# Kernel tuning notes

Hardware: AMD Instinct MI355X
Metric: run time of the kernel (lower is better)

The kernel has to match this reference:

```python
import jax, jax.numpy as jnp
import numpy as np

VOCAB, DIM, SEQ, DEPTH, WS, MULT = 32, 256, 8192, 6, 512, 4
BATCH = 2
NEG = -1e9  # mask fill value


def setup_inputs():
    key = jax.random.key(0)
    ks = jax.random.split(key, 8)
    L, d, h = DEPTH, DIM, DIM * MULT
    s = 0.02
    return {
        "tokens": jax.random.randint(ks[0], (BATCH, SEQ), 0, VOCAB),
        "embed": jax.random.normal(ks[1], (VOCAB, d)) * s,
        "ff_ln_s": jnp.ones((L, d)),
        "ff_ln_b": jnp.zeros((L, d)),
        "w1": jax.random.normal(ks[2], (L, d, h)) * s,
        "b1": jnp.zeros((L, h)),
        "w2": jax.random.normal(ks[3], (L, h, d)) * s,
        "b2": jnp.zeros((L, d)),
        "lnf_s": jnp.ones((d,)),
        "lnf_b": jnp.zeros((d,)),
        "w_out": jax.random.normal(ks[4], (d, VOCAB)) * s,
        "b_out": jnp.zeros((VOCAB,)),
    }


def layer_norm(x, s, b, eps=1e-5):
    m = jnp.mean(x, axis=-1, keepdims=True)
    v = jnp.var(x, axis=-1, keepdims=True)
    return (x - m) * jax.lax.rsqrt(v + eps) * s + b


def rotate_half(x):
    x1, x2 = jnp.split(x, 2, axis=-1)
    return jnp.concatenate([-x2, x1], axis=-1)


def local_attn(x, ws):
    # lucidrains LocalAttention: causal, look_backward=1, look_forward=0,
    # exact_windowsize=True, rotary pos emb on q/k. q = k = v = x (no projections).
    b, n, d = x.shape
    inv_freq = 1.0 / (10000.0 ** (jnp.arange(0, d, 2, dtype=jnp.float32) / d))
    t = jnp.arange(n, dtype=jnp.float32)
    fr = t[:, None] * inv_freq[None, :]
    fr = jnp.concatenate([fr, fr], axis=-1)  # (n, d)
    qk = x * jnp.cos(fr) + rotate_half(x) * jnp.sin(fr)  # rotary applied to q and k (identical)
    w = n // ws
    bq = qk.reshape(b, w, ws, d)
    bk = bq  # q == k here
    bv = x.reshape(b, w, ws, d)
    # look_around: each window sees [previous window, current window]
    pk = jnp.pad(bk, ((0, 0), (1, 0), (0, 0), (0, 0)))[:, :-1]
    pv = jnp.pad(bv, ((0, 0), (1, 0), (0, 0), (0, 0)))[:, :-1]
    bk2 = jnp.concatenate([pk, bk], axis=2)  # (b, w, 2*ws, d)
    bv2 = jnp.concatenate([pv, bv], axis=2)
    tq = jnp.arange(n).reshape(w, ws)
    tp = jnp.pad(tq, ((1, 0), (0, 0)), constant_values=-1)[:-1]
    tk = jnp.concatenate([tp, tq], axis=1)  # (w, 2*ws), -1 marks pad
    allowed = (
        (tk[:, None, :] >= 0)
        & (tq[:, :, None] >= tk[:, None, :])          # causal
        & (tq[:, :, None] <= tk[:, None, :] + ws)     # exact windowsize (look_backward=1)
    )
    sim = jnp.einsum("bwid,bwjd->bwij", bq, bk2) * (d ** -0.5)
    sim = jnp.where(allowed[None], sim, NEG)
    attn = jax.nn.softmax(sim, axis=-1)
    out = jnp.einsum("bwij,bwjd->bwid", attn, bv2)
    return out.reshape(b, n, d)


def reference(tokens, embed, ff_ln_s, ff_ln_b, w1, b1, w2, b2, lnf_s, lnf_b, w_out, b_out):
    x = embed[tokens]  # (b, n, d)
    for i in range(DEPTH):
        x = x + local_attn(x, WS)
        h = layer_norm(x, ff_ln_s[i], ff_ln_b[i])
        h = jax.nn.gelu(h @ w1[i] + b1[i], approximate=False)
        x = x + (h @ w2[i] + b2[i])
    return layer_norm(x, lnf_s, lnf_b) @ w_out + b_out  # (b, n, vocab)
```

## Files before the change

### kernel.cpp

```cpp
#include <hip/hip_runtime.h>
#include <hip/hip_bf16.h>
#include <math.h>

#define BATCH 2
#define SEQL 8192
#define DD 256
#define HDIM 1024
#define NLAYER 6
#define WSZ 512
#define NVOCAB 32
#define NTOK (BATCH*SEQL)
#define PLN (DD*HDIM)

typedef unsigned short u16;
typedef __attribute__((ext_vector_type(8))) short bf16x8;
typedef __attribute__((ext_vector_type(4))) float f32x4;

union B8 { uint4 u; bf16x8 b; ushort s[8]; uint w[4]; };

__device__ inline float bf2f(u16 v){
  unsigned int u = ((unsigned int)v) << 16;
  return __uint_as_float(u);
}
__device__ inline u16 f2bf(float f){
  unsigned int u = __float_as_uint(f);
  u += 0x7fff + ((u >> 16) & 1);
  return (u16)(u >> 16);
}

__device__ __forceinline__ void gload16(const void* g, void* l){
  __builtin_amdgcn_global_load_lds(
      (const __attribute__((address_space(1))) unsigned int*)g,
      (__attribute__((address_space(3))) unsigned int*)l, 16, 0, 0);
}

__global__ void k_tables(float* __restrict__ ct, float* __restrict__ st){
  int idx = blockIdx.x * 256 + threadIdx.x;
  if (idx >= SEQL * 128) return;
  int t = idx >> 7, i = idx & 127;
  float freq = expf(-((float)i / 128.0f) * 9.210340371976184f);
  float fr = (float)t * freq;
  ct[idx] = cosf(fr);
  st[idx] = sinf(fr);
}

__global__ void k_embed(const int* __restrict__ tokens, const float* __restrict__ emb,
                        float* __restrict__ x){
  int idx = blockIdx.x * 256 + threadIdx.x;
  int bt = idx >> 6, dv = (idx & 63) << 2;
  int tok = tokens[bt];
  *(float4*)(x + bt * DD + dv) = *(const float4*)(emb + tok * DD + dv);
}

__global__ void k_rope(const float* __restrict__ x, const float* __restrict__ ct,
                       const float* __restrict__ st, u16* __restrict__ qk,
                       u16* __restrict__ xv){
  int idx = blockIdx.x * 256 + threadIdx.x;
  int bt = idx >> 5, iv = (idx & 31) << 2;
  int t = bt & (SEQL - 1);
  const float* xr = x + bt * DD;
  float4 x1 = *(const float4*)(xr + iv);
  float4 x2 = *(const float4*)(xr + 128 + iv);
  float4 c = *(const float4*)(ct + t * 128 + iv);
  float4 s = *(const float4*)(st + t * 128 + iv);
  ushort4 q1, q2, v1, v2;
  q1.x = f2bf(x1.x * c.x - x2.x * s.x);  q2.x = f2bf(x2.x * c.x + x1.x * s.x);
  q1.y = f2bf(x1.y * c.y - x2.y * s.y);  q2.y = f2bf(x2.y * c.y + x1.y * s.y);
  q1.z = f2bf(x1.z * c.z - x2.z * s.z);  q2.z = f2bf(x2.z * c.z + x1.z * s.z);
  q1.w = f2bf(x1.w * c.w - x2.w * s.w);  q2.w = f2bf(x2.w * c.w + x1.w * s.w);
  v1.x = f2bf(x1.x); v1.y = f2bf(x1.y); v1.z = f2bf(x1.z); v1.w = f2bf(x1.w);
  v2.x = f2bf(x2.x); v2.y = f2bf(x2.y); v2.z = f2bf(x2.z); v2.w = f2bf(x2.w);
  *(ushort4*)(qk + bt * DD + iv)       = q1;
  *(ushort4*)(qk + bt * DD + 128 + iv) = q2;
  *(ushort4*)(xv + bt * DD + iv)       = v1;
  *(ushort4*)(xv + bt * DD + 128 + iv) = v2;
}

__global__ void __launch_bounds__(512, 2) k_attn2(const u16* __restrict__ qk,
                                                  const u16* __restrict__ xv,
                                                  const float* __restrict__ x,
                                                  float* __restrict__ y,
                                                  const float* __restrict__ g,
                                                  const float* __restrict__ b,
                                                  u16* __restrict__ lnx,
                                                  int fuse){
  __shared__ char smem[131072];
  float* redbuf = (float*)smem;

  const int tid = threadIdx.x;
  const int lane = tid & 63;
  const int w = tid >> 6;
  const int qh = w >> 1, kh = w & 1;
  const int l15 = lane & 15, lg = lane >> 4;

  const int qg = (blockIdx.x & 7) * 32 + (blockIdx.x >> 3);
  const int qb = qg * 64;
  const int t0 = qb & (SEQL - 1);
  const size_t bbase = (size_t)(qb >> 13) << 13;

  uint4 qf[8];
  {
    const u16* qr = qk + (size_t)(qb + qh*16 + l15) * DD + lg*4;
    #pragma unroll
    for (int s = 0; s < 8; ++s){
      uint2 a = *(const uint2*)(qr + s*32);
      uint2 bq = *(const uint2*)(qr + s*32 + 16);
      qf[s] = make_uint4(a.x, a.y, bq.x, bq.y);
    }
  }

  f32x4 oacc[16];
  #pragma unroll
  for (int d = 0; d < 16; ++d) oacc[d] = (f32x4){0.f, 0.f, 0.f, 0.f};
  float lacc = 0.f;

  const int p0 = (t0 >= WSZ) ? (t0 - WSZ) : 0;
  const int ntile = ((t0 - p0) >> 6) + 1;

  const int sk15 = tid & 15, skt = (tid >> 4) & 3, sc = tid >> 6;
  const int sdh = tid & 31, sk0 = (tid >> 5) * 4;
  const int vkhw = sk0 >> 5, vh = (sk0 >> 4) & 1, vlgw = (sk0 >> 2) & 3;

  uint4 kreg[4];
  uint  vreg[4][4];

  {
    const u16* sb = qk + (bbase + (size_t)p0 + skt*16 + sk15) * DD;
    #pragma unroll
    for (int u = 0; u < 4; ++u) kreg[u] = *(const uint4*)(sb + u*64 + sc*8);
    #pragma unroll
    for (int u = 0; u < 4; ++u){
      int d0 = sdh*2 + u*64;
      const u16* vb = xv + (bbase + (size_t)p0 + sk0) * DD + d0;
      vreg[u][0] = *(const uint*)(vb);
      vreg[u][1] = *(const uint*)(vb + DD);
      vreg[u][2] = *(const uint*)(vb + 2*DD);
      vreg[u][3] = *(const uint*)(vb + 3*DD);
    }
  }
  #pragma unroll
  for (int u = 0; u < 4; ++u){
    int d0 = u*64 + sc*8;
    int s = d0 >> 5, r = d0 & 31;
    int h = r >> 4, lgw = (r & 15) >> 2;
    int rec = ((s*4 + skt)*4 + lgw)*16 + sk15;
    char* wp = smem + rec*16 + h*8;
    *(uint2*)wp         = make_uint2(kreg[u].x, kreg[u].y);
    *(uint2*)(wp + 256) = make_uint2(kreg[u].z, kreg[u].w);
  }
  #pragma unroll
  for (int u = 0; u < 4; ++u){
    int d0 = sdh*2 + u*64;
    uint a0 = vreg[u][0], a1 = vreg[u][1], a2 = vreg[u][2], a3 = vreg[u][3];
    uint w0 = (a0 & 0xffffu) | (a1 << 16);
    uint w1 = (a2 & 0xffffu) | (a3 << 16);
    uint w2 = (a0 >> 16) | (a1 & 0xffff0000u);
    uint w3 = (a2 >> 16) | (a3 & 0xffff0000u);
    int dimt = d0 >> 4, d15 = d0 & 15;
    int rec = ((dimt*2 + vkhw)*4 + vlgw)*16 + d15;
    char* wp = smem + 32768 + rec*16 + vh*8;
    *(uint2*)wp        = make_uint2(w0, w1);
    *(uint2*)(wp + 16) = make_uint2(w2, w3);
  }
  __syncthreads();

  int cur = 0;
  for (int ti = 0; ti < ntile; ++ti){
    const int p = p0 + ti*64;
    if (ti + 1 < ntile){
      const int pn = p + 64;
      const u16* sb = qk + (bbase + (size_t)pn + skt*16 + sk15) * DD;
      #pragma unroll
      for (int u = 0; u < 4; ++u) kreg[u] = *(const uint4*)(sb + u*64 + sc*8);
      #pragma unroll
      for (int u = 0; u < 4; ++u){
        int d0 = sdh*2 + u*64;
        const u16* vb = xv + (bbase + (size_t)pn + sk0) * DD + d0;
        vreg[u][0] = *(const uint*)(vb);
        vreg[u][1] = *(const uint*)(vb + DD);
        vreg[u][2] = *(const uint*)(vb + 2*DD);
        vreg[u][3] = *(const uint*)(vb + 3*DD);
      }
    }

    char* Klds = smem + cur*65536;
    char* Vlds = Klds + 32768;

    f32x4 sacc[2];
    sacc[0] = (f32x4){0.f,0.f,0.f,0.f};
    sacc[1] = (f32x4){0.f,0.f,0.f,0.f};
    #pragma unroll
    for (int s = 0; s < 8; ++s){
      B8 ka0, ka1, qbf;
      ka0.b = *(const bf16x8*)(Klds + (((s*4 + kh*2+0)*4 + lg)*16 + l15)*16);
      ka1.b = *(const bf16x8*)(Klds + (((s*4 + kh*2+1)*4 + lg)*16 + l15)*16);
      qbf.u = qf[s];
      sacc[0] = __builtin_amdgcn_mfma_f32_16x16x32_bf16(ka0.b, qbf.b, sacc[0], 0, 0, 0);
      sacc[1] = __builtin_amdgcn_mfma_f32_16x16x32_bf16(ka1.b, qbf.b, sacc[1], 0, 0, 0);
    }

    B8 pa;
    #pragma unroll
    for (int ktp = 0; ktp < 2; ++ktp){
      int kbase = p + kh*32 + ktp*16 + lg*4;
      int qpos = t0 + qh*16 + l15;
      #pragma unroll
      for (int r = 0; r < 4; ++r){
        int kpos = kbase + r;
        float sv = sacc[ktp][r] * 0.0625f;
        bool ok = (kpos <= qpos) && (qpos <= kpos + WSZ);
        float pv = ok ? __expf(sv) : 0.0f;
        lacc += pv;
        pa.s[ktp*4 + r] = f2bf(pv);
      }
    }

    #pragma unroll
    for (int dimt = 0; dimt < 16; ++dimt){
      B8 vb;
      vb.b = *(const bf16x8*)(Vlds + (((dimt*2 + kh)*4 + lg)*16 + l15)*16);
      oacc[dimt] = __builtin_amdgcn_mfma_f32_16x16x32_bf16(pa.b, vb.b, oacc[dimt], 0, 0, 0);
    }

    if (ti + 1 < ntile){
      char* nK = smem + (cur ^ 1)*65536;
      char* nV = nK + 32768;
      #pragma unroll
      for (int u = 0; u < 4; ++u){
        int d0 = u*64 + sc*8;
        int s = d0 >> 5, r = d0 & 31;
        int h = r >> 4, lgw = (r & 15) >> 2;
        int rec = ((s*4 + skt)*4 + lgw)*16 + sk15;
        char* wp = nK + rec*16 + h*8;
        *(uint2*)wp         = make_uint2(kreg[u].x, kreg[u].y);
        *(uint2*)(wp + 256) = make_uint2(kreg[u].z, kreg[u].w);
      }
      #pragma unroll
      for (int u = 0; u < 4; ++u){
        int d0 = sdh*2 + u*64;
        uint a0 = vreg[u][0], a1 = vreg[u][1], a2 = vreg[u][2], a3 = vreg[u][3];
        uint w0 = (a0 & 0xffffu) | (a1 << 16);
        uint w1 = (a2 & 0xffffu) | (a3 << 16);
        uint w2 = (a0 >> 16) | (a1 & 0xffff0000u);
        uint w3 = (a2 >> 16) | (a3 & 0xffff0000u);
        int dimt = d0 >> 4, d15 = d0 & 15;
        int rec = ((dimt*2 + vkhw)*4 + vlgw)*16 + d15;
        char* wp = nV + rec*16 + vh*8;
        *(uint2*)wp        = make_uint2(w0, w1);
        *(uint2*)(wp + 16) = make_uint2(w2, w3);
      }
    }
    __syncthreads();
    cur ^= 1;
  }

  lacc += __shfl_xor(lacc, 16, 64);
  lacc += __shfl_xor(lacc, 32, 64);
  if (lane < 16) redbuf[kh*64 + qh*16 + l15] = lacc;
  __syncthreads();
  if (tid < 64) redbuf[128 + tid] = redbuf[tid] + redbuf[64 + tid];
  __syncthreads();

  const int q = tid >> 3, dv = (tid & 7) * 4;
  float4 ovs[8];
  float lsum = 0.f, lss = 0.f;

  float* opass = redbuf + 192;
  #pragma unroll
  for (int pass = 0; pass < 8; ++pass){
    #pragma unroll
    for (int dt = 0; dt < 2; ++dt){
      int dimt = pass*2 + dt;
      #pragma unroll
      for (int r = 0; r < 4; ++r){
        int qrow = qh*16 + lg*4 + r;
        opass[(kh*64 + qrow)*36 + dt*16 + l15] = oacc[dimt][r];
      }
    }
    __syncthreads();
    {
      float4 o0 = *(float4*)&opass[q*36 + dv];
      float4 o1 = *(float4*)&opass[(64 + q)*36 + dv];
      float inv = 1.0f / redbuf[128 + q];
      size_t gi = (size_t)(qb + q) * DD + pass*32 + dv;
      float4 xr = *(const float4*)(x + gi);
      float4 ov;
      ov.x = xr.x + (o0.x + o1.x) * inv;
      ov.y = xr.y + (o0.y + o1.y) * inv;
      ov.z = xr.z + (o0.z + o1.z) * inv;
      ov.w = xr.w + (o0.w + o1.w) * inv;
      *(float4*)(y + gi) = ov;
      ovs[pass] = ov;
      lsum += ov.x + ov.y + ov.z + ov.w;
      lss  += ov.x*ov.x + ov.y*ov.y + ov.z*ov.z + ov.w*ov.w;
    }
    __syncthreads();
  }

  if (fuse){
    #pragma unroll
    for (int o = 1; o < 8; o <<= 1){
      lsum += __shfl_xor(lsum, o, 64);
      lss  += __shfl_xor(lss,  o, 64);
    }
    float m = lsum * (1.0f / DD);
    float var = lss * (1.0f / DD) - m * m;
    float rs = rsqrtf(var + 1e-5f);
    #pragma unroll
    for (int pass = 0; pass < 8; ++pass){
      float4 gf = *(const float4*)(g + pass*32 + dv);
      float4 bf = *(const float4*)(b + pass*32 + dv);
      ushort4 o4;
      o4.x = f2bf((ovs[pass].x - m) * rs * gf.x + bf.x);
      o4.y = f2bf((ovs[pass].y - m) * rs * gf.y + bf.y);
      o4.z = f2bf((ovs[pass].z - m) * rs * gf.z + bf.z);
      o4.w = f2bf((ovs[pass].w - m) * rs * gf.w + bf.w);
      *(ushort4*)(lnx + (size_t)(qb + q) * DD + pass*32 + dv) = o4;
    }
  }
}

__global__ void __launch_bounds__(256) k_ln(const float* __restrict__ in,
                                            const float* __restrict__ g,
                                            const float* __restrict__ b,
                                            u16* __restrict__ out){
  int wid = (blockIdx.x * 256 + threadIdx.x) >> 6;
  int lane = threadIdx.x & 63;
  float4 v = *(const float4*)(in + wid * DD + lane * 4);
  float s = v.x + v.y + v.z + v.w;
  float ss = v.x * v.x + v.y * v.y + v.z * v.z + v.w * v.w;
  #pragma unroll
  for (int o = 32; o; o >>= 1){ s += __shfl_xor(s, o, 64); ss += __shfl_xor(ss, o, 64); }
  float m = s * (1.0f / DD);
  float var = ss * (1.0f / DD) - m * m;
  float rs = rsqrtf(var + 1e-5f);
  float4 gf = *(const float4*)(g + lane * 4);
  float4 bf = *(const float4*)(b + lane * 4);
  ushort4 o4;
  o4.x = f2bf((v.x - m) * rs * gf.x + bf.x);
  o4.y = f2bf((v.y - m) * rs * gf.y + bf.y);
  o4.z = f2bf((v.z - m) * rs * gf.z + bf.z);
  o4.w = f2bf((v.w - m) * rs * gf.w + bf.w);
  *(ushort4*)(out + wid * DD + lane * 4) = o4;
}

template<int KDIM, int NDIM>
__device__ __forceinline__ void split_one(const float* __restrict__ W,
                                          u16* __restrict__ Phi, int idx){
  int c15 = idx & 15;
  int lg = (idx >> 4) & 3;
  int nt = (idx >> 6) % (NDIM/16);
  int ks = idx / ((NDIM/16) * 64);
  int col = nt*16 + c15;
  B8 hi;
  #pragma unroll
  for (int j = 0; j < 8; ++j){
    int k = ks*32 + (j >> 2)*16 + lg*4 + (j & 3);
    hi.s[j] = f2bf(W[(size_t)k * NDIM + col]);
  }
  *(uint4*)(Phi + (size_t)idx * 8) = hi.u;
}

__global__ void __launch_bounds__(256) k_split2(const float* __restrict__ W1,
                                                const float* __restrict__ W2,
                                                u16* __restrict__ P){
  int b = blockIdx.x;
  if (b < 128) split_one<DD, HDIM>(W1, P, b*256 + threadIdx.x);
  else         split_one<HDIM, DD>(W2, P + PLN, (b - 128)*256 + threadIdx.x);
}

template<int KDIM, int NDIM, int EPI>
__global__ void __launch_bounds__(256, 4) k_gemm(const u16* __restrict__ A,
                                              const u16* __restrict__ BhG,
                                              const float* __restrict__ bias,
                                              const float* __restrict__ res,
                                              float* __restrict__ outf,
                                              u16* __restrict__ outh){
  __shared__ char smem[18432 + 8192];
  char* As = smem;
  char* Bs = smem + 18432;

  const int tid = threadIdx.x;
  const int lane = tid & 63;
  const int w = tid >> 6;
  const int wr = w >> 1, wc = w & 1;
  const int l15 = lane & 15, lg = lane >> 4;
  const int m0 = blockIdx.y * 128;
  const int n0 = blockIdx.x * 64;
  const int NT16 = NDIM / 16;

  f32x4 acc[4][2];
  #pragma unroll
  for (int a = 0; a < 4; ++a){
    acc[a][0] = (f32x4){0.f,0.f,0.f,0.f};
    acc[a][1] = (f32x4){0.f,0.f,0.f,0.f};
  }

  for (int kb = 0; kb < KDIM/64; ++kb){
    __syncthreads();
    #pragma unroll
    for (int p = 0; p < 4; ++p){
      int c = p*256 + tid;
      int row = c >> 3, cc = c & 7;
      uint4 v = *(const uint4*)(A + (size_t)(m0 + row) * KDIM + kb*64 + cc*8);
      *(uint4*)(As + row*144 + cc*16) = v;
    }
    #pragma unroll
    for (int p = 0; p < 2; ++p){
      int j = p*256 + tid;
      int chunk = j >> 6, r = j & 63;
      const u16* src = BhG
          + (((size_t)(kb*2 + (chunk >> 2)) * NT16 + (n0 >> 4) + (chunk & 3))*64 + r)*8;
      gload16(src, Bs + j*16);
    }
    __syncthreads();

    #pragma unroll
    for (int s = 0; s < 2; ++s){
      B8 af[4], bhf[2];
      #pragma unroll
      for (int a = 0; a < 4; ++a){
        const char* ab = As + (wr*64 + a*16 + l15)*144 + s*64 + lg*8;
        uint2 lo = *(const uint2*)ab;
        uint2 hi = *(const uint2*)(ab + 32);
        af[a].u = make_uint4(lo.x, lo.y, hi.x, hi.y);
      }
      #pragma unroll
      for (int c = 0; c < 2; ++c){
        int off = (((s*4 + wc*2 + c)*64) + lg*16 + l15)*16;
        bhf[c].u = *(const uint4*)(Bs + off);
      }
      #pragma unroll
      for (int a = 0; a < 4; ++a)
        #pragma unroll
        for (int c = 0; c < 2; ++c)
          acc[a][c] = __builtin_amdgcn_mfma_f32_16x16x32_bf16(af[a].b, bhf[c].b, acc[a][c], 0, 0, 0);
    }
  }

  float bv[2];
  bv[0] = bias[n0 + wc*32 + l15];
  bv[1] = bias[n0 + wc*32 + 16 + l15];

  #pragma unroll
  for (int a = 0; a < 4; ++a){
    #pragma unroll
    for (int c = 0; c < 2; ++c){
      #pragma unroll
      for (int r = 0; r < 4; ++r){
        int row = m0 + wr*64 + a*16 + lg*4 + r;
        int col = n0 + wc*32 + c*16 + l15;
        float v = acc[a][c][r] + bv[c];
        if (EPI == 0){
          float gl = 0.5f * v * (1.0f + erff(v * 0.70710678f));
          outh[(size_t)row * NDIM + col] = f2bf(gl);
        } else {
          outf[(size_t)row * NDIM + col] = v + res[(size_t)row * NDIM + col];
        }
      }
    }
  }
}

__global__ void __launch_bounds__(256) k_final(const float* __restrict__ x,
                                               const float* __restrict__ g,
                                               const float* __restrict__ b,
                                               const float* __restrict__ wout,
                                               const float* __restrict__ bout,
                                               float* __restrict__ out){
  __shared__ float lds[4][256];
  int widx = threadIdx.x >> 6, lane = threadIdx.x & 63;
  int bt = blockIdx.x * 4 + widx;
  float4 v = *(const float4*)(x + bt * DD + lane * 4);
  float s = v.x + v.y + v.z + v.w;
  float ss = v.x * v.x + v.y * v.y + v.z * v.z + v.w * v.w;
  #pragma unroll
  for (int o = 32; o; o >>= 1){ s += __shfl_xor(s, o, 64); ss += __shfl_xor(ss, o, 64); }
  float m = s * (1.0f / DD);
  float var = ss * (1.0f / DD) - m * m;
  float rs = rsqrtf(var + 1e-5f);
  float4 gf = *(const float4*)(g + lane * 4);
  float4 bf = *(const float4*)(b + lane * 4);
  lds[widx][lane * 4 + 0] = (v.x - m) * rs * gf.x + bf.x;
  lds[widx][lane * 4 + 1] = (v.y - m) * rs * gf.y + bf.y;
  lds[widx][lane * 4 + 2] = (v.z - m) * rs * gf.z + bf.z;
  lds[widx][lane * 4 + 3] = (v.w - m) * rs * gf.w + bf.w;
  __syncthreads();
  int vo = lane & 31, half = lane >> 5;
  const float* lp = &lds[widx][half * 128];
  const float* wp = wout + half * 128 * NVOCAB + vo;
  float acc = 0;
  #pragma unroll 4
  for (int d = 0; d < 128; ++d) acc += lp[d] * wp[d * NVOCAB];
  acc += __shfl_down(acc, 32, 64);
  if (lane < 32) out[bt * NVOCAB + vo] = acc + bout[vo];
}

extern "C" void kernel_launch(void* const* d_in, const int* in_sizes, int n_in,
                              void* d_out, int out_size, void* d_ws, size_t ws_size,
                              hipStream_t stream) {
  const int*   tokens = (const int*)d_in[0];
  const float* emb   = (const float*)d_in[1];
  const float* ffs   = (const float*)d_in[2];
  const float* ffb   = (const float*)d_in[3];
  const float* w1    = (const float*)d_in[4];
  const float* b1    = (const float*)d_in[5];
  const float* w2    = (const float*)d_in[6];
  const float* b2    = (const float*)d_in[7];
  const float* lnfs  = (const float*)d_in[8];
  const float* lnfb  = (const float*)d_in[9];
  const float* wout  = (const float*)d_in[10];
  const float* bout  = (const float*)d_in[11];
  float* out = (float*)d_out;

  char* ws = (char*)d_ws;
  float* x    = (float*)(ws);
  float* y    = (float*)(ws + (size_t)16*1024*1024);
  u16*   buf8 = (u16*)  (ws + (size_t)32*1024*1024);
  u16*   qk   = (u16*)  (ws + (size_t)40*1024*1024);
  u16*   h    = (u16*)  (ws + (size_t)48*1024*1024);
  float* ct   = (float*)(ws + (size_t)80*1024*1024);
  float* st   = (float*)(ws + (size_t)84*1024*1024);

  const int fuse = (ws_size >= (size_t)96*1024*1024) ? 1 : 0;
  u16* lnx = fuse ? (u16*)(ws + (size_t)88*1024*1024)
                  : buf8;

  k_tables<<<4096, 256, 0, stream>>>(ct, st);
  k_embed<<<4096, 256, 0, stream>>>(tokens, emb, x);
  for (int L = 0; L < NLAYER; ++L){
    k_rope<<<2048, 256, 0, stream>>>(x, ct, st, qk, buf8);
    k_attn2<<<256, 512, 0, stream>>>(qk, buf8, x, y,
                                     ffs + L*DD, ffb + L*DD, lnx, fuse);
    if (!fuse)
      k_ln<<<4096, 256, 0, stream>>>(y, ffs + L*DD, ffb + L*DD, lnx);
    k_split2<<<256, 256, 0, stream>>>(w1 + (size_t)L*PLN, w2 + (size_t)L*PLN, qk);
    k_gemm<DD, HDIM, 0><<<dim3(16, 128), 256, 0, stream>>>(
        lnx, qk, b1 + L*HDIM, nullptr, nullptr, h);
    k_gemm<HDIM, DD, 1><<<dim3(4, 128), 256, 0, stream>>>(
        h, qk + PLN, b2 + L*DD, y, x, nullptr);
  }
  k_final<<<4096, 256, 0, stream>>>(x, lnfs, lnfb, wout, bout, out);
}
```

Measured before the change: 711.5 us.

## Fuse FFN GEMMs into one kernel keeping hidden activations in registers

Replaces the two separate FFN GEMM kernels with a single fused kernel. Each wave holds a 16-token tile, computes the hidden activations chunk by chunk with GELU applied in registers, and feeds them straight into the second matmul, so the bf16 hidden tensor never goes to global memory. Weight pre-splitting for all layers is hoisted into one launch before the layer loop. In exchange, weight fragments are read directly from global memory with no LDS sharing, which puts heavy weight traffic through L2. Only 256 blocks are launched, which limits occupancy on a large GPU.

```diff
diff --git a/kernel.cpp b/kernel.cpp
--- a/kernel.cpp
+++ b/kernel.cpp
@@ -26,12 +26,6 @@
   unsigned int u = __float_as_uint(f);
   u += 0x7fff + ((u >> 16) & 1);
   return (u16)(u >> 16);
-}
-
-__device__ __forceinline__ void gload16(const void* g, void* l){
-  __builtin_amdgcn_global_load_lds(
-      (const __attribute__((address_space(1))) unsigned int*)g,
-      (__attribute__((address_space(3))) unsigned int*)l, 16, 0, 0);
 }
 
 __global__ void k_tables(float* __restrict__ ct, float* __restrict__ st){
@@ -361,103 +355,88 @@
   *(uint4*)(Phi + (size_t)idx * 8) = hi.u;
 }
 
-__global__ void __launch_bounds__(256) k_split2(const float* __restrict__ W1,
-                                                const float* __restrict__ W2,
-                                                u16* __restrict__ P){
-  int b = blockIdx.x;
-  if (b < 128) split_one<DD, HDIM>(W1, P, b*256 + threadIdx.x);
-  else         split_one<HDIM, DD>(W2, P + PLN, (b - 128)*256 + threadIdx.x);
-}
-
-template<int KDIM, int NDIM, int EPI>
-__global__ void __launch_bounds__(256, 4) k_gemm(const u16* __restrict__ A,
-                                              const u16* __restrict__ BhG,
-                                              const float* __restrict__ bias,
-                                              const float* __restrict__ res,
-                                              float* __restrict__ outf,
-                                              u16* __restrict__ outh){
-  __shared__ char smem[18432 + 8192];
-  char* As = smem;
-  char* Bs = smem + 18432;
-
+__global__ void __launch_bounds__(256) k_splitall(const float* __restrict__ w1,
+                                                  const float* __restrict__ w2,
+                                                  u16* __restrict__ P){
+  int bk = blockIdx.x;
+  int L = bk >> 8, r = bk & 255;
+  u16* PL = P + (size_t)L * 2 * PLN;
+  if (r < 128) split_one<DD, HDIM>(w1 + (size_t)L*PLN, PL, r*256 + threadIdx.x);
+  else         split_one<HDIM, DD>(w2 + (size_t)L*PLN, PL + PLN, (r-128)*256 + threadIdx.x);
+}
+
+__global__ void __launch_bounds__(256) k_ffn(const u16* __restrict__ lnx,
+                                             const u16* __restrict__ P1,
+                                             const u16* __restrict__ P2,
+                                             const float* __restrict__ b1,
+                                             const float* __restrict__ b2,
+                                             const float* __restrict__ y,
+                                             float* __restrict__ x){
   const int tid = threadIdx.x;
   const int lane = tid & 63;
   const int w = tid >> 6;
-  const int wr = w >> 1, wc = w & 1;
   const int l15 = lane & 15, lg = lane >> 4;
-  const int m0 = blockIdx.y * 128;
-  const int n0 = blockIdx.x * 64;
-  const int NT16 = NDIM / 16;
-
-  f32x4 acc[4][2];
-  #pragma unroll
-  for (int a = 0; a < 4; ++a){
-    acc[a][0] = (f32x4){0.f,0.f,0.f,0.f};
-    acc[a][1] = (f32x4){0.f,0.f,0.f,0.f};
-  }
-
-  for (int kb = 0; kb < KDIM/64; ++kb){
-    __syncthreads();
-    #pragma unroll
-    for (int p = 0; p < 4; ++p){
-      int c = p*256 + tid;
-      int row = c >> 3, cc = c & 7;
-      uint4 v = *(const uint4*)(A + (size_t)(m0 + row) * KDIM + kb*64 + cc*8);
-      *(uint4*)(As + row*144 + cc*16) = v;
-    }
-    #pragma unroll
-    for (int p = 0; p < 2; ++p){
-      int j = p*256 + tid;
-      int chunk = j >> 6, r = j & 63;
-      const u16* src = BhG
-          + (((size_t)(kb*2 + (chunk >> 2)) * NT16 + (n0 >> 4) + (chunk & 3))*64 + r)*8;
-      gload16(src, Bs + j*16);
-    }
-    __syncthreads();
-
-    #pragma unroll
-    for (int s = 0; s < 2; ++s){
-      B8 af[4], bhf[2];
-      #pragma unroll
-      for (int a = 0; a < 4; ++a){
-        const char* ab = As + (wr*64 + a*16 + l15)*144 + s*64 + lg*8;
-        uint2 lo = *(const uint2*)ab;
-        uint2 hi = *(const uint2*)(ab + 32);
-        af[a].u = make_uint4(lo.x, lo.y, hi.x, hi.y);
-      }
-      #pragma unroll
-      for (int c = 0; c < 2; ++c){
-        int off = (((s*4 + wc*2 + c)*64) + lg*16 + l15)*16;
-        bhf[c].u = *(const uint4*)(Bs + off);
-      }
-      #pragma unroll
-      for (int a = 0; a < 4; ++a)
-        #pragma unroll
-        for (int c = 0; c < 2; ++c)
-          acc[a][c] = __builtin_amdgcn_mfma_f32_16x16x32_bf16(af[a].b, bhf[c].b, acc[a][c], 0, 0, 0);
-    }
-  }
-
-  float bv[2];
-  bv[0] = bias[n0 + wc*32 + l15];
-  bv[1] = bias[n0 + wc*32 + 16 + l15];
-
-  #pragma unroll
-  for (int a = 0; a < 4; ++a){
-    #pragma unroll
-    for (int c = 0; c < 2; ++c){
+  const int tok0 = blockIdx.x * 64 + w * 16;
+
+  uint4 xf[8];
+  {
+    const u16* ar = lnx + (size_t)(tok0 + l15) * DD + lg * 4;
+    #pragma unroll
+    for (int s = 0; s < 8; ++s){
+      uint2 a = *(const uint2*)(ar + s*32);
+      uint2 bq = *(const uint2*)(ar + s*32 + 16);
+      xf[s] = make_uint4(a.x, a.y, bq.x, bq.y);
+    }
+  }
+
+  f32x4 acc[16];
+  #pragma unroll
+  for (int d = 0; d < 16; ++d) acc[d] = (f32x4){0.f,0.f,0.f,0.f};
+
+  for (int nc = 0; nc < 16; ++nc){
+    f32x4 hacc[4];
+    #pragma unroll
+    for (int hb = 0; hb < 4; ++hb) hacc[hb] = (f32x4){0.f,0.f,0.f,0.f};
+    #pragma unroll
+    for (int s = 0; s < 8; ++s){
+      B8 xb; xb.u = xf[s];
+      #pragma unroll
+      for (int hb = 0; hb < 4; ++hb){
+        B8 wa;
+        wa.u = *(const uint4*)(P1 + (((size_t)((s*64 + nc*4 + hb)*4 + lg)*16 + l15))*8);
+        hacc[hb] = __builtin_amdgcn_mfma_f32_16x16x32_bf16(wa.b, xb.b, hacc[hb], 0, 0, 0);
+      }
+    }
+    B8 pa0, pa1;
+    #pragma unroll
+    for (int hb = 0; hb < 4; ++hb){
       #pragma unroll
       for (int r = 0; r < 4; ++r){
-        int row = m0 + wr*64 + a*16 + lg*4 + r;
-        int col = n0 + wc*32 + c*16 + l15;
-        float v = acc[a][c][r] + bv[c];
-        if (EPI == 0){
-          float gl = 0.5f * v * (1.0f + erff(v * 0.70710678f));
-          outh[(size_t)row * NDIM + col] = f2bf(gl);
-        } else {
-          outf[(size_t)row * NDIM + col] = v + res[(size_t)row * NDIM + col];
-        }
-      }
+        float v = hacc[hb][r] + b1[nc*64 + hb*16 + lg*4 + r];
+        float gl = 0.5f * v * (1.0f + erff(v * 0.70710678f));
+        if (hb < 2) pa0.s[hb*4 + r] = f2bf(gl);
+        else        pa1.s[(hb-2)*4 + r] = f2bf(gl);
+      }
+    }
+    #pragma unroll
+    for (int ks2 = 0; ks2 < 2; ++ks2){
+      #pragma unroll
+      for (int dcb = 0; dcb < 16; ++dcb){
+        B8 wb;
+        wb.u = *(const uint4*)(P2 + (((size_t)(((nc*2+ks2)*16 + dcb)*4 + lg)*16 + l15))*8);
+        acc[dcb] = __builtin_amdgcn_mfma_f32_16x16x32_bf16(
+            ks2 ? pa1.b : pa0.b, wb.b, acc[dcb], 0, 0, 0);
+      }
+    }
+  }
+
+  #pragma unroll
+  for (int dcb = 0; dcb < 16; ++dcb){
+    float bv = b2[dcb*16 + l15];
+    #pragma unroll
+    for (int r = 0; r < 4; ++r){
+      size_t gi = (size_t)(tok0 + lg*4 + r) * DD + dcb*16 + l15;
+      x[gi] = acc[dcb][r] + bv + y[gi];
     }
   }
 }
@@ -518,27 +497,26 @@
   float* y    = (float*)(ws + (size_t)16*1024*1024);
   u16*   buf8 = (u16*)  (ws + (size_t)32*1024*1024);
   u16*   qk   = (u16*)  (ws + (size_t)40*1024*1024);
-  u16*   h    = (u16*)  (ws + (size_t)48*1024*1024);
+  u16*   pln  = (u16*)  (ws + (size_t)48*1024*1024);
   float* ct   = (float*)(ws + (size_t)80*1024*1024);
   float* st   = (float*)(ws + (size_t)84*1024*1024);
 
   const int fuse = (ws_size >= (size_t)96*1024*1024) ? 1 : 0;
   u16* lnx = fuse ? (u16*)(ws + (size_t)88*1024*1024)
-                  : buf8;
+                  : (u16*)(ws + (size_t)56*1024*1024);
 
   k_tables<<<4096, 256, 0, stream>>>(ct, st);
   k_embed<<<4096, 256, 0, stream>>>(tokens, emb, x);
+  k_splitall<<<1536, 256, 0, stream>>>(w1, w2, pln);
   for (int L = 0; L < NLAYER; ++L){
     k_rope<<<2048, 256, 0, stream>>>(x, ct, st, qk, buf8);
     k_attn2<<<256, 512, 0, stream>>>(qk, buf8, x, y,
                                      ffs + L*DD, ffb + L*DD, lnx, fuse);
     if (!fuse)
       k_ln<<<4096, 256, 0, stream>>>(y, ffs + L*DD, ffb + L*DD, lnx);
-    k_split2<<<256, 256, 0, stream>>>(w1 + (size_t)L*PLN, w2 + (size_t)L*PLN, qk);
-    k_gemm<DD, HDIM, 0><<<dim3(16, 128), 256, 0, stream>>>(
-        lnx, qk, b1 + L*HDIM, nullptr, nullptr, h);
-    k_gemm<HDIM, DD, 1><<<dim3(4, 128), 256, 0, stream>>>(
-        h, qk + PLN, b2 + L*DD, y, x, nullptr);
+    k_ffn<<<256, 256, 0, stream>>>(lnx, pln + (size_t)L*2*PLN,
+                                   pln + (size_t)L*2*PLN + PLN,
+                                   b1 + L*HDIM, b2 + L*DD, y, x);
   }
   k_final<<<4096, 256, 0, stream>>>(x, lnfs, lnfb, wout, bout, out);
 }
```

New measurement: 2.052 ms. 188% more time.
